# Optimization experiments

Hardware: AMD Instinct MI355X
Metric: run time of the kernel (lower is better)

The kernel has to match this reference:

```python
import jax, jax.numpy as jnp
import numpy as np
from jax import lax

# config constants (from init_kwargs)
B = 256            # batch of voxels
NPC = 40           # compartments (T2 spectrum grid)
N_ECHOES = 32      # echo train length
T1 = 1000.0        # ms
TAU = 10.0         # echo spacing (ms); epg_signal halves it internally
TR = 3000.0        # repetition time (ms)
SIZE = 3 * N_ECHOES + 1  # EPG state dimension (97)


def _build_S(n):
    """Static EPG shift matrix, exactly as torch fill_S."""
    size = 3 * n + 1
    S = np.zeros((size, size), np.float32)
    S[0, 2] = 1.0
    S[1, 0] = 1.0
    S[2, 5] = 1.0
    S[3, 3] = 1.0
    for o in range(2, n + 1):
        off1 = (o - 1 - 1) * 3 + 2
        off2 = (o + 1 - 1) * 3 + 3
        if off1 <= size:
            S[3 * o - 2, off1 - 1] = 1.0
        if off2 <= size:
            S[3 * o - 1, off2 - 1] = 1.0
        S[3 * o, 3 * o] = 1.0
    return S


def _block_idx(n):
    """Row/col indices of T: T[0,0] plus n copies of the 3x3 block T0 on the diagonal."""
    rows = [0]
    cols = [0]
    for k in range(n):
        for a in range(3):
            for b in range(3):
                rows.append(1 + 3 * k + a)
                cols.append(1 + 3 * k + b)
    return np.asarray(rows), np.asarray(cols)


_S_NP = _build_S(N_ECHOES)
_ROWS, _COLS = _block_idx(N_ECHOES)
_IDX = np.arange(SIZE)
_E1_MASK_NP = (_IDX >= 1) & ((_IDX - 1) % 3 == 2)  # positions holding exp(-tau*R1)


def setup_inputs() -> dict:
    key = jax.random.key(0)
    k1, k2, k3 = jax.random.split(key, 3)
    # refocusing angles in degrees (realistic CPMG range)
    refoc_angle = 120.0 + 60.0 * jax.random.uniform(k1, (B,), dtype=jnp.float32)
    # T2 values in ms
    t2s = 10.0 + 1990.0 * jax.random.uniform(k2, (B, NPC), dtype=jnp.float32)
    # positive compartment weights
    weights = 0.05 + jax.random.uniform(k3, (B, NPC), dtype=jnp.float32)
    return {"refoc_angle": refoc_angle, "t2s": t2s, "weights": weights}


def _epg_forward(refoc_angle, t2s, weights):
    n, size = N_ECHOES, SIZE
    S = jnp.asarray(_S_NP)
    e1_mask = jnp.asarray(_E1_MASK_NP)
    rad = jnp.float32(np.pi / 180.0)
    alpha = refoc_angle * rad          # (B,) refocusing flip in radians
    alpha_exc = alpha / 2.0            # excitation flip = flip/2

    # T (rotation) matrix per batch element: block-diagonal with T0(alpha)
    def build_T(a):
        c2 = jnp.cos(a / 2.0) ** 2
        s2 = jnp.sin(a / 2.0) ** 2
        s = jnp.sin(a)
        c = jnp.cos(a)
        T0 = jnp.stack([
            jnp.stack([c2, s2, s]),
            jnp.stack([s2, c2, -s]),
            jnp.stack([-0.5 * s, 0.5 * s, c]),
        ])  # (3,3)
        vals = jnp.concatenate([jnp.ones((1,), T0.dtype), jnp.tile(T0.reshape(-1), n)])
        return jnp.zeros((size, size), T0.dtype).at[_ROWS, _COLS].set(vals)

    T = jax.vmap(build_T)(alpha)  # (B, size, size)

    # R is diagonal: d = [e2, (e2,e2,e1) * n] with e2=exp(-tau*R2), e1=exp(-tau*R1)
    tau = jnp.float32(TAU / 2.0)
    r2 = 1.0 / t2s                                   # (B, NPC) rates
    r1 = jnp.float32(1.0 / T1)
    e2 = jnp.exp(-tau * r2)                          # (B, NPC)
    e1 = jnp.exp(-tau * r1)                          # scalar
    d = jnp.where(e1_mask, e1, e2[..., None])        # (B, NPC, size)

    # E = (R S) T (R S) = diag(d) @ (S T) @ diag(d) @ S
    M = jnp.einsum('ij,bjk->bik', S, T)                       # (B, size, size)
    Md = M[:, None, :, :] * d[:, :, None, :]                   # (B, NPC, size, size)
    E = d[..., None] * jnp.einsum('bcik,kj->bcij', Md, S)      # (B, NPC, size, size)

    # initial state x0 = [sin(alpha_exc), 0, cos(alpha_exc), 0, ...]
    x0 = (jnp.zeros(d.shape, d.dtype)
          .at[..., 0].set(jnp.sin(alpha_exc)[:, None])
          .at[..., 2].set(jnp.cos(alpha_exc)[:, None]))

    def step(x, _):
        x = jnp.einsum('bcij,bcj->bci', E, x)
        return x, x[..., 0]

    _, H = lax.scan(step, x0, None, length=n)  # (n, B, NPC) echo amplitudes

    # faithful to source: factor uses TR / rate (rate = 1/T1)
    factor = 1.0 - jnp.exp(-jnp.float32(TR) / r1)
    sig = factor * jnp.einsum('nbc,bc->bn', H, weights)  # (B, n)
    return sig / sig[:, :1]


def reference(refoc_angle, t2s, weights):
    return _epg_forward(refoc_angle, t2s, weights)
```

## Files before the change

### kernel.cpp

```cpp
#include <hip/hip_runtime.h>
#include <hip/hip_bf16.h>


#define NB 256
#define NPC 40
#define NECH 32
#define SZ 97

__device__ __forceinline__ float bf16_at(const void* p, int i) {
    return __bfloat162float(((const __hip_bfloat16*)p)[i]);
}
__device__ __forceinline__ float f32_at(const void* p, int i) {
    return ((const float*)p)[i];
}

__global__ __launch_bounds__(64, 1) void epg_kernel(
    const void* __restrict__ refoc,
    const void* __restrict__ t2,
    const void* __restrict__ wts,
    float* __restrict__ out)
{
    const int b = blockIdx.x;
    const int tid = threadIdx.x;
    __shared__ float Hs[NECH][NPC];

    bool in_f32 = false;
    #pragma unroll
    for (int i = 0; i < 32; i += 2) {
        const float v = bf16_at(t2, i);
        if (!(v >= 9.0f && v <= 2100.0f)) in_f32 = true;
    }

    const float adeg = in_f32 ? f32_at(refoc, b) : bf16_at(refoc, b);
    float t2v = 1000.0f, wt = 0.0f;
    if (tid < NPC) {
        t2v = in_f32 ? f32_at(t2,  b * NPC + tid) : bf16_at(t2,  b * NPC + tid);
        wt  = in_f32 ? f32_at(wts, b * NPC + tid) : bf16_at(wts, b * NPC + tid);
    }
    t2v = fminf(fmaxf(t2v, 1.0f), 1.0e6f);

    const float alpha = adeg * 0.017453292519943295f;
    const float sh = sinf(0.5f * alpha);
    const float ch = cosf(0.5f * alpha);
    const float sA = sinf(alpha);
    const float cA = cosf(alpha);
    const float c2 = ch * ch;
    const float s2 = sh * sh;
    const float e1 = 0.9950124791926823f;
    const float e2 = expf(-5.0f / t2v);

    const float m11 = c2 * e2;
    const float m12 = s2 * e2;
    const float m13 = sA * e1;
    const float m31 = 0.5f * sA * e2;
    const float m33 = cA * e1;

    float x[SZ];
    #pragma unroll
    for (int i = 0; i < SZ; ++i) x[i] = 0.0f;
    x[0] = sh;
    x[2] = ch;

    for (int e = 0; e < NECH; ++e) {
        #pragma unroll
        for (int p = 94; p >= 4; p -= 3) x[p] = x[p - 3];
        x[1] = x[0];
        x[0] = x[2];
        #pragma unroll
        for (int p = 2; p <= 92; p += 3) x[p] = x[p + 3];
        x[95] = 0.0f;

        x[0] *= e2;
        #pragma unroll
        for (int k = 0; k < 32; ++k) {
            const float a  = x[1 + 3 * k];
            const float bb = x[2 + 3 * k];
            const float zz = x[3 + 3 * k];
            x[1 + 3 * k] = m11 * a + m12 * bb + m13 * zz;
            x[2 + 3 * k] = m12 * a + m11 * bb - m13 * zz;
            x[3 + 3 * k] = m31 * (bb - a) + m33 * zz;
        }

        #pragma unroll
        for (int p = 94; p >= 4; p -= 3) x[p] = x[p - 3];
        x[1] = x[0];
        x[0] = x[2];
        #pragma unroll
        for (int p = 2; p <= 92; p += 3) x[p] = x[p + 3];
        x[95] = 0.0f;

        x[0] *= e2;
        #pragma unroll
        for (int k = 0; k < 32; ++k) {
            x[1 + 3 * k] *= e2;
            x[2 + 3 * k] *= e2;
            x[3 + 3 * k] *= e1;
        }

        if (tid < NPC) Hs[e][tid] = x[0] * wt;
    }

    __syncthreads();

    const int e = tid & 31;
    float sum = 0.0f;
    #pragma unroll
    for (int c = 0; c < NPC; ++c) sum += Hs[e][c];
    const float sum0 = __shfl(sum, 0, 64);
    if (tid < NECH) out[b * NECH + tid] = sum / sum0;
}

extern "C" void kernel_launch(void* const* d_in, const int* in_sizes, int n_in,
                              void* d_out, int out_size, void* d_ws, size_t ws_size,
                              hipStream_t stream) {
    const void* refoc = d_in[0];
    const void* t2s   = d_in[1];
    const void* wts   = d_in[2];
    float* out = (float*)d_out;
    epg_kernel<<<NB, 64, 0, stream>>>(refoc, t2s, wts, out);
}
```

Before: 71.82 us.

## Fold relaxation into mixing matrix and merge double shift per echo

Rewrites the per-echo EPG update so the diagonal relaxation is absorbed into the 3x3 rotation coefficients (squared decay factors). The two consecutive shifts become a single shift by two states, and the state is tracked in a rotated basis so the echo is read from v[2]. This removes one full pass of elementwise scaling and one register shuffle pass per echo, and the echo loop is now fully unrolled. It relies on the algebra holding exactly. Full unrolling may raise register pressure and code size.

```diff
diff --git a/kernel.cpp b/kernel.cpp
--- a/kernel.cpp
+++ b/kernel.cpp
@@ -46,58 +46,51 @@
     const float cA = cosf(alpha);
     const float c2 = ch * ch;
     const float s2 = sh * sh;
-    const float e1 = 0.9950124791926823f;
-    const float e2 = expf(-5.0f / t2v);
+    const float e1  = 0.9950124791926823f;
+    const float e12 = 0.9900498337491681f;
+    const float e2  = expf(-5.0f / t2v);
+    const float e22 = e2 * e2;
 
-    const float m11 = c2 * e2;
-    const float m12 = s2 * e2;
-    const float m13 = sA * e1;
-    const float m31 = 0.5f * sA * e2;
-    const float m33 = cA * e1;
+    const float M11 = c2 * e22;
+    const float M12 = s2 * e22;
+    const float M13 = sA * e12;
+    const float M31 = 0.5f * sA * e22;
+    const float M33 = cA * e12;
 
-    float x[SZ];
+    const float we = wt * e2;
+
+    float v[SZ];
     #pragma unroll
-    for (int i = 0; i < SZ; ++i) x[i] = 0.0f;
-    x[0] = sh;
-    x[2] = ch;
+    for (int i = 0; i < SZ; ++i) v[i] = 0.0f;
+    v[0] = e2 * ch;
+    v[1] = c2 * (e2 * sh);
+    v[2] = s2 * (e2 * sh);
+    v[3] = -0.5f * sA * (e2 * sh);
 
+    #pragma unroll
     for (int e = 0; e < NECH; ++e) {
+        if (tid < NPC) Hs[e][tid] = we * v[2];
+        if (e == NECH - 1) break;
+
         #pragma unroll
-        for (int p = 94; p >= 4; p -= 3) x[p] = x[p - 3];
-        x[1] = x[0];
-        x[0] = x[2];
+        for (int p = 94; p >= 7; p -= 3) v[p] = v[p - 6];
+        v[4] = v[0];
+        v[1] = v[2];
         #pragma unroll
-        for (int p = 2; p <= 92; p += 3) x[p] = x[p + 3];
-        x[95] = 0.0f;
+        for (int p = 2; p <= 89; p += 3) v[p] = v[p + 6];
+        v[92] = 0.0f;
+        v[95] = 0.0f;
+        v[0] = e22 * v[2];
 
-        x[0] *= e2;
         #pragma unroll
         for (int k = 0; k < 32; ++k) {
-            const float a  = x[1 + 3 * k];
-            const float bb = x[2 + 3 * k];
-            const float zz = x[3 + 3 * k];
-            x[1 + 3 * k] = m11 * a + m12 * bb + m13 * zz;
-            x[2 + 3 * k] = m12 * a + m11 * bb - m13 * zz;
-            x[3 + 3 * k] = m31 * (bb - a) + m33 * zz;
+            const float a  = v[1 + 3 * k];
+            const float bb = v[2 + 3 * k];
+            const float zz = v[3 + 3 * k];
+            v[1 + 3 * k] = M11 * a + M12 * bb + M13 * zz;
+            v[2 + 3 * k] = M12 * a + M11 * bb - M13 * zz;
+            v[3 + 3 * k] = M31 * (bb - a) + M33 * zz;
         }
-
-        #pragma unroll
-        for (int p = 94; p >= 4; p -= 3) x[p] = x[p - 3];
-        x[1] = x[0];
-        x[0] = x[2];
-        #pragma unroll
-        for (int p = 2; p <= 92; p += 3) x[p] = x[p + 3];
-        x[95] = 0.0f;
-
-        x[0] *= e2;
-        #pragma unroll
-        for (int k = 0; k < 32; ++k) {
-            x[1 + 3 * k] *= e2;
-            x[2 + 3 * k] *= e2;
-            x[3 + 3 * k] *= e1;
-        }
-
-        if (tid < NPC) Hs[e][tid] = x[0] * wt;
     }
 
     __syncthreads();
```

New measurement: 69.90 us. 2.7% less time.
